# Performance work log

Hardware: AMD Instinct MI355X
Metric: run time of the kernel (lower is better)

## Reference

```python
import jax, jax.numpy as jnp
import numpy as np

B, T, D, H = 2, 2048, 1024, 16
DK = D // H


def setup_inputs() -> dict:
    key = jax.random.key(0)
    ks = jax.random.split(key, 12)
    s = 0.02
    return {
        "query": jax.random.normal(ks[0], (B, T, D), jnp.float32),
        "key": jax.random.normal(ks[1], (B, T, D), jnp.float32),
        "value": jax.random.normal(ks[2], (B, T, D), jnp.float32),
        "mask": jax.random.randint(ks[3], (B, T), 0, 2) != 0,  # True = keep
        "Wq": jax.random.normal(ks[4], (D, D), jnp.float32) * s,
        "bq": jnp.zeros((D,), jnp.float32),
        "Wk": jax.random.normal(ks[5], (D, D), jnp.float32) * s,
        "bk": jnp.zeros((D,), jnp.float32),
        "Wv": jax.random.normal(ks[6], (D, D), jnp.float32) * s,
        "bv": jnp.zeros((D,), jnp.float32),
        "Wo": jax.random.normal(ks[7], (D, D), jnp.float32) * s,
        "bo": jnp.zeros((D,), jnp.float32),
    }


def _split_heads(x):
    # [B, S, D] -> [B, H, S, DK]
    b, s, _ = x.shape
    return x.reshape(b, s, H, DK).transpose(0, 2, 1, 3)


def reference(query, key, value, mask, Wq, bq, Wk, bk, Wv, bv, Wo, bo):
    # torch Linear: y = x @ W.T + b
    q = _split_heads(query @ Wq.T + bq)   # [B,H,T,DK]
    k = _split_heads(key @ Wk.T + bk)     # [B,H,S,DK]
    v = _split_heads(value @ Wv.T + bv)   # [B,H,S,DK]
    scale = 1.0 / np.sqrt(DK).astype(np.float32)
    scores = jnp.einsum('bhtd,bhsd->bhts', q, k) * scale  # [B,H,T,S]
    # key-padding mask [B,S] -> broadcast [B,1,1,S], True = keep
    scores = jnp.where(mask[:, None, None, :], scores, -jnp.inf)
    attn = jax.nn.softmax(scores, axis=-1)
    out = jnp.einsum('bhts,bhsd->bhtd', attn, v)           # [B,H,T,DK]
    out = out.transpose(0, 2, 1, 3).reshape(query.shape[0], -1, D)
    return out @ Wo.T + bo
```

## Files before the change

kernel.cpp:

```cpp
#include <hip/hip_runtime.h>
#include <stdint.h>

#define B_SZ 2
#define T_SEQ 2048
#define DMODEL 1024
#define NHEAD 16
#define DKH 64
#define M_ROWS (B_SZ * T_SEQ)

#define LDT 72

#define INP_E  4194304u
#define W_E    1048576u

typedef __bf16 bf16x8 __attribute__((ext_vector_type(8)));
typedef float  f32x4  __attribute__((ext_vector_type(4)));

__device__ __forceinline__ unsigned short f2bf(float f) {
    unsigned u = __builtin_bit_cast(unsigned, f);
    u += 0x7fffu + ((u >> 16) & 1u);
    return (unsigned short)(u >> 16);
}
__device__ __forceinline__ uint4 cvt8(const float* p) {
    float4 f0 = *(const float4*)p, f1 = *(const float4*)(p + 4);
    uint4 r;
    r.x = (unsigned)f2bf(f0.x) | ((unsigned)f2bf(f0.y) << 16);
    r.y = (unsigned)f2bf(f0.z) | ((unsigned)f2bf(f0.w) << 16);
    r.z = (unsigned)f2bf(f1.x) | ((unsigned)f2bf(f1.y) << 16);
    r.w = (unsigned)f2bf(f1.z) | ((unsigned)f2bf(f1.w) << 16);
    return r;
}

__device__ __forceinline__ void async16(const unsigned short* g, unsigned short* l) {
    __builtin_amdgcn_global_load_lds(
        (const __attribute__((address_space(1))) void*)g,
        (__attribute__((address_space(3))) void*)l, 16, 0, 0);
}
__device__ __forceinline__ void async4(const unsigned short* g, unsigned short* l) {
    __builtin_amdgcn_global_load_lds(
        (const __attribute__((address_space(1))) void*)g,
        (__attribute__((address_space(3))) void*)l, 4, 0, 0);
}

__global__ __launch_bounds__(256) void cvt_all(
    const float* __restrict__ q, const float* __restrict__ k, const float* __restrict__ v,
    const float* __restrict__ wq, const float* __restrict__ wk,
    const float* __restrict__ wv, const float* __restrict__ wo,
    unsigned short* __restrict__ wsb)
{
    int blk = blockIdx.x;
    const float* src; unsigned short* dst; int lb;
    if      (blk < 2048) { src = q;  dst = wsb;                       lb = blk; }
    else if (blk < 4096) { src = k;  dst = wsb + INP_E;               lb = blk - 2048; }
    else if (blk < 6144) { src = v;  dst = wsb + 2 * INP_E;           lb = blk - 4096; }
    else if (blk < 6656) { src = wq; dst = wsb + 3 * INP_E;           lb = blk - 6144; }
    else if (blk < 7168) { src = wk; dst = wsb + 3 * INP_E + W_E;     lb = blk - 6656; }
    else if (blk < 7680) { src = wv; dst = wsb + 3 * INP_E + 2 * W_E; lb = blk - 7168; }
    else                 { src = wo; dst = wsb + 3 * INP_E + 3 * W_E; lb = blk - 7680; }
    size_t i = ((size_t)lb * 256 + threadIdx.x) * 8;
    *(uint4*)&dst[i] = cvt8(src + i);
}

template<int C_MODE, int MT>
__device__ __forceinline__ void gemm_core(
    const unsigned short* __restrict__ A, const unsigned short* __restrict__ W,
    const float* __restrict__ bias, void* __restrict__ C,
    int N, int K, int bx, int by,
    unsigned short* sA, unsigned short* sB)
{
    const int tid  = threadIdx.x;
    const int wave = tid >> 6, lane = tid & 63;
    const int quad = lane >> 4, l15 = lane & 15;
    const int TM = MT * 32;
    const int m0 = by * TM, n0 = bx * 128;
    const int wm = (wave & 1) * (MT * 16), wn = (wave >> 1) * 64;

    f32x4 acc[MT][4] = {};

    for (int k0 = 0; k0 < K; k0 += 64) {
        __syncthreads();
        #pragma unroll
        for (int i = 0; i < MT; i++) {
            int c   = tid + 256 * i;
            int row = c >> 3;
            int gk  = ((c & 7) ^ (row & 7)) * 8;
            int sb  = (wave * 64 + 256 * i) * 8;
            async16(&A[(size_t)(m0 + row) * K + k0 + gk], sA + sb);
        }
        #pragma unroll
        for (int i = 0; i < 4; i++) {
            int c   = tid + 256 * i;
            int row = c >> 3;
            int gk  = ((c & 7) ^ (row & 7)) * 8;
            int sb  = (wave * 64 + 256 * i) * 8;
            async16(&W[(size_t)(n0 + row) * K + k0 + gk], sB + sb);
        }
        __syncthreads();
        const int sw = l15 & 7;
        #pragma unroll
        for (int ks = 0; ks < 2; ks++) {
            bf16x8 af[MT], bfv[4];
            #pragma unroll
            for (int mt = 0; mt < MT; mt++)
                af[mt] = *(const bf16x8*)&sA[(wm + mt * 16 + l15) * 64 +
                                             (((ks * 4 + quad) ^ sw) * 8)];
            #pragma unroll
            for (int nt = 0; nt < 4; nt++)
                bfv[nt] = *(const bf16x8*)&sB[(wn + nt * 16 + l15) * 64 +
                                              (((ks * 4 + quad) ^ sw) * 8)];
            #pragma unroll
            for (int mt = 0; mt < MT; mt++)
                #pragma unroll
                for (int nt = 0; nt < 4; nt++)
                    acc[mt][nt] = __builtin_amdgcn_mfma_f32_16x16x32_bf16(
                        af[mt], bfv[nt], acc[mt][nt], 0, 0, 0);
        }
    }

    if (C_MODE == 2) {
        #pragma unroll
        for (int mt = 0; mt < MT; mt++) {
            #pragma unroll
            for (int r = 0; r < 4; r++) {
                int m = m0 + wm + mt * 16 + quad * 4 + r;
                float bm = bias[m];
                #pragma unroll
                for (int nt = 0; nt < 4; nt++) {
                    int n = n0 + wn + nt * 16 + l15;
                    int bb = n >> 11, t = n & 2047;
                    ((unsigned short*)C)[((size_t)bb * 1024 + m) * 2048 + t] =
                        f2bf(acc[mt][nt][r] + bm);
                }
            }
        }
    } else {
        #pragma unroll
        for (int nt = 0; nt < 4; nt++) {
            int n = n0 + wn + nt * 16 + l15;
            float bv = bias[n];
            #pragma unroll
            for (int mt = 0; mt < MT; mt++) {
                #pragma unroll
                for (int r = 0; r < 4; r++) {
                    int m = m0 + wm + mt * 16 + quad * 4 + r;
                    float val = acc[mt][nt][r] + bv;
                    if (C_MODE == 1) ((float*)C)[(size_t)m * N + n] = val;
                    else ((unsigned short*)C)[(size_t)m * N + n] = f2bf(val);
                }
            }
        }
    }
}

__global__ __launch_bounds__(256) void gemm_qkv(
    const unsigned short* __restrict__ Qb, const unsigned short* __restrict__ Kb,
    const unsigned short* __restrict__ Vb,
    const unsigned short* __restrict__ Wqb, const unsigned short* __restrict__ Wkb,
    const unsigned short* __restrict__ Wvb,
    const float* __restrict__ bq, const float* __restrict__ bk, const float* __restrict__ bv,
    unsigned short* __restrict__ Qp, unsigned short* __restrict__ Kp,
    unsigned short* __restrict__ Vt)
{
    __shared__ __align__(16) unsigned short sA[128 * 64];
    __shared__ __align__(16) unsigned short sB[128 * 64];
    const int z = blockIdx.z, id = blockIdx.x;
    if (z < 2) {
        gemm_core<0, 4>(z ? Kb : Qb, z ? Wkb : Wqb, z ? bk : bq, z ? Kp : Qp,
                        DMODEL, DMODEL, id & 7, id >> 3, sA, sB);
    } else {
        gemm_core<2, 4>(Wvb, Vb, bv, Vt, M_ROWS, DMODEL, id & 31, id >> 5, sA, sB);
    }
}

__global__ __launch_bounds__(256) void gemm_o(
    const unsigned short* __restrict__ AO, const unsigned short* __restrict__ Wob,
    const float* __restrict__ bo, float* __restrict__ out)
{
    __shared__ __align__(16) unsigned short sA[64 * 64];
    __shared__ __align__(16) unsigned short sB[128 * 64];
    const int id = blockIdx.x;
    gemm_core<1, 2>(AO, Wob, bo, out, DMODEL, DMODEL, id & 7, id >> 3, sA, sB);
}

#define QBLK 128
#define KVB 64

__global__ __launch_bounds__(512, 4) void attn_kernel(
    const unsigned short* __restrict__ Qp,
    const unsigned short* __restrict__ Kp,
    const unsigned short* __restrict__ Vt,
    const int* __restrict__ maskp,
    unsigned short* __restrict__ Op)
{
    __shared__ __align__(16) unsigned char sMEM[73728];
    unsigned short* sK  = (unsigned short*)sMEM;
    unsigned short* sV  = (unsigned short*)(sMEM + 32768);
    float*          smf = (float*)(sMEM + 65536);

    const int tid  = threadIdx.x;
    const int wave = tid >> 6, lane = tid & 63;
    const int g    = wave >> 2, wl = wave & 3;
    const int quad = lane >> 4, l15 = lane & 15;
    const int qblk = blockIdx.x, h = blockIdx.y, b = blockIdx.z;

    const float SCL2 = 0.125f * 1.44269504089f;
    const float MNEG = -30000.f;

    bf16x8 aq[2][2];
    #pragma unroll
    for (int mt = 0; mt < 2; mt++) {
        const int qrow = qblk * QBLK + wl * 32 + mt * 16 + l15;
        const unsigned short* qptr =
            Qp + (size_t)(b * T_SEQ + qrow) * DMODEL + h * DKH + quad * 8;
        aq[mt][0] = *(const bf16x8*)qptr;
        aq[mt][1] = *(const bf16x8*)(qptr + 32);
    }

    const unsigned short* Kb_ = Kp + (size_t)b * T_SEQ * DMODEL + h * DKH;
    const unsigned short* VtB = Vt + ((size_t)b * DMODEL + h * DKH) * T_SEQ;

    int kOff[2], kSb[2];
    #pragma unroll
    for (int i = 0; i < 2; i++) {
        int c = tid + 512 * i;
        int tile = c >> 9, cc = c & 511;
        int row = cc >> 3;
        int gk = ((cc & 7) ^ (row & 7)) * 8;
        kOff[i] = (tile * 64 + row) * DMODEL + gk;
        kSb[i]  = (wave * 64 + 512 * i) * 8;
    }
    int vOff[8], vSb[8];
    #pragma unroll
    for (int i = 0; i < 8; i++) {
        int P    = wave * 2048 + i * 256 + lane * 4;
        int tile = P >> 13;
        int rp   = P & 8191;
        int row  = rp >> 7;
        int cb   = (rp >> 4) & 7;
        int slot = (rp >> 2) & 3;
        int c    = cb ^ (row & 7);
        int f    = c * 4 + slot;
        int g2   = ((f >> 4) << 1) | ((f >> 1) & 1);
        int qq   = (f >> 2) & 3;
        int r2   = (f & 1) * 2;
        int keyoff = g2 * 16 + qq * 4 + r2;
        vOff[i] = row * T_SEQ + tile * 64 + keyoff;
        vSb[i]  = (wave * 2048 + i * 256) >> 1;
    }

    f32x4 O[2][4] = {};
    float l_r[2] = {0.f, 0.f};

    #pragma unroll
    for (int i = 0; i < 2; i++)
        async16(&Kb_[kOff[i]], sK + kSb[i]);
    #pragma unroll
    for (int i = 0; i < 8; i++)
        async4(&VtB[vOff[i]], sV + vSb[i]);
    #pragma unroll
    for (int j = 0; j < 4; j++) {
        int i = tid + 512 * j;
        smf[i] = maskp[b * T_SEQ + i] ? 0.f : MNEG;
    }
    __syncthreads();

    const int sw = l15 & 7;
    for (int rr = 0; rr < T_SEQ / (2 * KVB); ++rr) {
        const int cur = rr & 1;
        if (rr + 1 < T_SEQ / (2 * KVB)) {
            const int nb = cur ^ 1;
            #pragma unroll
            for (int i = 0; i < 2; i++)
                async16(&Kb_[(size_t)(rr + 1) * 128 * DMODEL + kOff[i]],
                        sK + nb * 8192 + kSb[i]);
            #pragma unroll
            for (int i = 0; i < 8; i++)
                async4(&VtB[(size_t)(rr + 1) * 128 + vOff[i]],
                       sV + nb * 8192 + vSb[i]);
        }

        const unsigned short* sKp = sK + cur * 8192 + g * 4096;
        const unsigned short* sVp = sV + cur * 8192 + g * 4096;
        const int s0 = (2 * rr + g) * KVB;

        f32x4 ST[2][4];
        __builtin_amdgcn_s_setprio(1);
        #pragma unroll
        for (int kt = 0; kt < 4; kt++) {
            const unsigned short* kr = &sKp[(kt * 16 + l15) * 64];
            const bf16x8 kf0 = *(const bf16x8*)&kr[(quad ^ sw) * 8];
            const bf16x8 kf1 = *(const bf16x8*)&kr[((quad + 4) ^ sw) * 8];
            #pragma unroll
            for (int mt = 0; mt < 2; mt++) {
                f32x4 z = {};
                z = __builtin_amdgcn_mfma_f32_16x16x32_bf16(kf0, aq[mt][0], z, 0, 0, 0);
                z = __builtin_amdgcn_mfma_f32_16x16x32_bf16(kf1, aq[mt][1], z, 0, 0, 0);
                ST[mt][kt] = z;
            }
        }
        __builtin_amdgcn_s_setprio(0);

        bf16x8 pb[2][2];
        #pragma unroll
        for (int kt = 0; kt < 4; kt++) {
            float4 m4 = *(const float4*)&smf[s0 + kt * 16 + quad * 4];
            float ma[4] = {m4.x, m4.y, m4.z, m4.w};
            #pragma unroll
            for (int mt = 0; mt < 2; mt++) {
                #pragma unroll
                for (int r = 0; r < 4; r++) {
                    float p = __builtin_amdgcn_exp2f(fmaf(ST[mt][kt][r], SCL2, ma[r]));
                    l_r[mt] += p;
                    pb[mt][kt >> 1][(kt & 1) * 4 + r] = (__bf16)p;
                }
            }
        }

        __builtin_amdgcn_s_setprio(1);
        #pragma unroll
        for (int nt = 0; nt < 4; nt++) {
            const unsigned short* vr = &sVp[(nt * 16 + l15) * 64];
            const bf16x8 vf0 = *(const bf16x8*)&vr[(quad ^ sw) * 8];
            const bf16x8 vf1 = *(const bf16x8*)&vr[((quad + 4) ^ sw) * 8];
            #pragma unroll
            for (int mt = 0; mt < 2; mt++) {
                O[mt][nt] = __builtin_amdgcn_mfma_f32_16x16x32_bf16(
                    vf0, pb[mt][0], O[mt][nt], 0, 0, 0);
                O[mt][nt] = __builtin_amdgcn_mfma_f32_16x16x32_bf16(
                    vf1, pb[mt][1], O[mt][nt], 0, 0, 0);
            }
        }
        __builtin_amdgcn_s_setprio(0);

        __syncthreads();
    }

    #pragma unroll
    for (int mt = 0; mt < 2; mt++) {
        float l = l_r[mt];
        l += __shfl_xor(l, 16);
        l += __shfl_xor(l, 32);
        l_r[mt] = l;
    }

    float* OM = (float*)sMEM;
    float* LM = (float*)(sMEM + 33280);
    if (g == 1) {
        #pragma unroll
        for (int mt = 0; mt < 2; mt++) {
            int row = wl * 32 + mt * 16 + l15;
            if (quad == 0) LM[row] = l_r[mt];
            #pragma unroll
            for (int nt = 0; nt < 4; nt++)
                #pragma unroll
                for (int r = 0; r < 4; r++)
                    OM[row * 65 + nt * 16 + quad * 4 + r] = O[mt][nt][r];
        }
    }
    __syncthreads();
    if (g == 0) {
        #pragma unroll
        for (int mt = 0; mt < 2; mt++) {
            int row = wl * 32 + mt * 16 + l15;
            float inv = 1.0f / fmaxf(l_r[mt] + LM[row], 1e-30f);
            int qg = qblk * QBLK + row;
            unsigned short* op = Op + (size_t)(b * T_SEQ + qg) * DMODEL + h * DKH;
            #pragma unroll
            for (int nt = 0; nt < 4; nt++) {
                ushort4 w;
                w.x = f2bf((O[mt][nt][0] + OM[row * 65 + nt * 16 + quad * 4 + 0]) * inv);
                w.y = f2bf((O[mt][nt][1] + OM[row * 65 + nt * 16 + quad * 4 + 1]) * inv);
                w.z = f2bf((O[mt][nt][2] + OM[row * 65 + nt * 16 + quad * 4 + 2]) * inv);
                w.w = f2bf((O[mt][nt][3] + OM[row * 65 + nt * 16 + quad * 4 + 3]) * inv);
                *(ushort4*)&op[nt * 16 + quad * 4] = w;
            }
        }
    }
}

template<int A_BF16, int W_BF16, int C_MODE>
__global__ __launch_bounds__(256) void gemm_bt_cvt(
    const void* __restrict__ A_, const void* __restrict__ W_,
    const float* __restrict__ bias, void* __restrict__ C_,
    int M, int N, int K)
{
    __shared__ __align__(16) unsigned short sA[128 * LDT];
    __shared__ __align__(16) unsigned short sB[128 * LDT];
    const int tid  = threadIdx.x;
    const int wave = tid >> 6, lane = tid & 63;
    const int quad = lane >> 4, l15 = lane & 15;
    const int m0 = blockIdx.y * 128, n0 = blockIdx.x * 128;
    const int wm = (wave & 1) * 64, wn = (wave >> 1) * 64;
    f32x4 acc[4][4] = {};
    for (int k0 = 0; k0 < K; k0 += 64) {
        __syncthreads();
        #pragma unroll
        for (int i = 0; i < 4; i++) {
            int c = tid + 256 * i;
            int row = c >> 3, koff = (c & 7) * 8;
            if (A_BF16)
                *(uint4*)&sA[row * LDT + koff] =
                    *(const uint4*)&((const unsigned short*)A_)[(size_t)(m0 + row) * K + k0 + koff];
            else
                *(uint4*)&sA[row * LDT + koff] =
                    cvt8((const float*)A_ + (size_t)(m0 + row) * K + k0 + koff);
            if (W_BF16)
                *(uint4*)&sB[row * LDT + koff] =
                    *(const uint4*)&((const unsigned short*)W_)[(size_t)(n0 + row) * K + k0 + koff];
            else
                *(uint4*)&sB[row * LDT + koff] =
                    cvt8((const float*)W_ + (size_t)(n0 + row) * K + k0 + koff);
        }
        __syncthreads();
        #pragma unroll
        for (int ks = 0; ks < 2; ks++) {
            bf16x8 af[4], bfr[4];
            #pragma unroll
            for (int mt = 0; mt < 4; mt++)
                af[mt] = *(const bf16x8*)&sA[(wm + mt * 16 + l15) * LDT + ks * 32 + quad * 8];
            #pragma unroll
            for (int nt = 0; nt < 4; nt++)
                bfr[nt] = *(const bf16x8*)&sB[(wn + nt * 16 + l15) * LDT + ks * 32 + quad * 8];
            #pragma unroll
            for (int mt = 0; mt < 4; mt++)
                #pragma unroll
                for (int nt = 0; nt < 4; nt++)
                    acc[mt][nt] = __builtin_amdgcn_mfma_f32_16x16x32_bf16(
                        af[mt], bfr[nt], acc[mt][nt], 0, 0, 0);
        }
    }
    if (C_MODE == 2) {
        #pragma unroll
        for (int mt = 0; mt < 4; mt++)
            #pragma unroll
            for (int r = 0; r < 4; r++) {
                int m = m0 + wm + mt * 16 + quad * 4 + r;
                float bm = bias[m];
                #pragma unroll
                for (int nt = 0; nt < 4; nt++) {
                    int n = n0 + wn + nt * 16 + l15;
                    int bb = n >> 11, t = n & 2047;
                    ((unsigned short*)C_)[((size_t)bb * 1024 + m) * 2048 + t] =
                        f2bf(acc[mt][nt][r] + bm);
                }
            }
    } else {
        #pragma unroll
        for (int nt = 0; nt < 4; nt++) {
            int n = n0 + wn + nt * 16 + l15;
            float bv = bias[n];
            #pragma unroll
            for (int mt = 0; mt < 4; mt++)
                #pragma unroll
                for (int r = 0; r < 4; r++) {
                    int m = m0 + wm + mt * 16 + quad * 4 + r;
                    float val = acc[mt][nt][r] + bv;
                    if (C_MODE == 1) ((float*)C_)[(size_t)m * N + n] = val;
                    else ((unsigned short*)C_)[(size_t)m * N + n] = f2bf(val);
                }
        }
    }
}

extern "C" void kernel_launch(void* const* d_in, const int* in_sizes, int n_in,
                              void* d_out, int out_size, void* d_ws, size_t ws_size,
                              hipStream_t stream)
{
    const float* q  = (const float*)d_in[0];
    const float* k  = (const float*)d_in[1];
    const float* v  = (const float*)d_in[2];
    const int*   mk = (const int*)d_in[3];
    const float* Wq = (const float*)d_in[4];
    const float* bq = (const float*)d_in[5];
    const float* Wk = (const float*)d_in[6];
    const float* bk = (const float*)d_in[7];
    const float* Wv = (const float*)d_in[8];
    const float* bv = (const float*)d_in[9];
    const float* Wo = (const float*)d_in[10];
    const float* bo = (const float*)d_in[11];
    float* out = (float*)d_out;

    unsigned short* wsb = (unsigned short*)d_ws;
    const dim3 gA(T_SEQ / QBLK, NHEAD, B_SZ);

    if (ws_size >= (size_t)64 * 1024 * 1024) {
        unsigned short* Qb  = wsb;
        unsigned short* Kb  = wsb + INP_E;
        unsigned short* Vb  = wsb + 2 * INP_E;
        unsigned short* Wqb = wsb + 3 * INP_E;
        unsigned short* Wkb = wsb + 3 * INP_E + W_E;
        unsigned short* Wvb = wsb + 3 * INP_E + 2 * W_E;
        unsigned short* Wob = wsb + 3 * INP_E + 3 * W_E;
        unsigned short* Qp  = wsb + 4 * INP_E;
        unsigned short* Kp  = wsb + 5 * INP_E;
        unsigned short* Vt  = wsb + 6 * INP_E;
        unsigned short* AO  = wsb + 7 * INP_E;

        cvt_all<<<8192, 256, 0, stream>>>(q, k, v, Wq, Wk, Wv, Wo, wsb);
        gemm_qkv<<<dim3(256, 1, 3), 256, 0, stream>>>(
            Qb, Kb, Vb, Wqb, Wkb, Wvb, bq, bk, bv, Qp, Kp, Vt);
        attn_kernel<<<gA, 512, 0, stream>>>(Qp, Kp, Vt, mk, AO);
        gemm_o<<<dim3(512, 1, 1), 256, 0, stream>>>(AO, Wob, bo, out);
    } else {
        unsigned short* Qp = wsb;
        unsigned short* Kp = wsb + INP_E;
        unsigned short* Vt = wsb + 2 * INP_E;
        unsigned short* AO = wsb + 3 * INP_E;
        const dim3 gN(DMODEL / 128, M_ROWS / 128);
        const dim3 gV(M_ROWS / 128, DMODEL / 128);
        gemm_bt_cvt<0, 0, 0><<<gN, 256, 0, stream>>>(q, Wq, bq, Qp, M_ROWS, DMODEL, DMODEL);
        gemm_bt_cvt<0, 0, 0><<<gN, 256, 0, stream>>>(k, Wk, bk, Kp, M_ROWS, DMODEL, DMODEL);
        gemm_bt_cvt<0, 0, 2><<<gV, 256, 0, stream>>>(Wv, v, bv, Vt, DMODEL, M_ROWS, DMODEL);
        attn_kernel<<<gA, 512, 0, stream>>>(Qp, Kp, Vt, mk, AO);
        gemm_bt_cvt<1, 0, 1><<<gN, 256, 0, stream>>>(AO, Wo, bo, out, M_ROWS, DMODEL, DMODEL);
    }
}
```

Baseline: 223.6 us.

## Widen attention block to 16 waves with four KV groups, single-buffered tiles

```diff
diff --git a/kernel.cpp b/kernel.cpp
--- a/kernel.cpp
+++ b/kernel.cpp
@@ -185,7 +185,7 @@
 #define QBLK 128
 #define KVB 64
 
-__global__ __launch_bounds__(512, 4) void attn_kernel(
+__global__ __launch_bounds__(1024, 8) void attn_kernel(
     const unsigned short* __restrict__ Qp,
     const unsigned short* __restrict__ Kp,
     const unsigned short* __restrict__ Vt,
@@ -222,30 +222,31 @@
     int kOff[2], kSb[2];
     #pragma unroll
     for (int i = 0; i < 2; i++) {
-        int c = tid + 512 * i;
+        int c = tid + 1024 * i;
         int tile = c >> 9, cc = c & 511;
         int row = cc >> 3;
         int gk = ((cc & 7) ^ (row & 7)) * 8;
         kOff[i] = (tile * 64 + row) * DMODEL + gk;
-        kSb[i]  = (wave * 64 + 512 * i) * 8;
+        kSb[i]  = (wave * 64 + 1024 * i) * 8;
     }
     int vOff[8], vSb[8];
     #pragma unroll
     for (int i = 0; i < 8; i++) {
-        int P    = wave * 2048 + i * 256 + lane * 4;
+        int c    = tid + 1024 * i;
+        int P    = c * 4;
         int tile = P >> 13;
         int rp   = P & 8191;
         int row  = rp >> 7;
         int cb   = (rp >> 4) & 7;
         int slot = (rp >> 2) & 3;
-        int c    = cb ^ (row & 7);
-        int f    = c * 4 + slot;
+        int cc2  = cb ^ (row & 7);
+        int f    = cc2 * 4 + slot;
         int g2   = ((f >> 4) << 1) | ((f >> 1) & 1);
         int qq   = (f >> 2) & 3;
         int r2   = (f & 1) * 2;
         int keyoff = g2 * 16 + qq * 4 + r2;
         vOff[i] = row * T_SEQ + tile * 64 + keyoff;
-        vSb[i]  = (wave * 2048 + i * 256) >> 1;
+        vSb[i]  = (wave * 64 + 1024 * i) * 2;
     }
 
     f32x4 O[2][4] = {};
@@ -258,30 +259,18 @@
     for (int i = 0; i < 8; i++)
         async4(&VtB[vOff[i]], sV + vSb[i]);
     #pragma unroll
-    for (int j = 0; j < 4; j++) {
-        int i = tid + 512 * j;
+    for (int j = 0; j < 2; j++) {
+        int i = tid + 1024 * j;
         smf[i] = maskp[b * T_SEQ + i] ? 0.f : MNEG;
     }
     __syncthreads();
 
     const int sw = l15 & 7;
-    for (int rr = 0; rr < T_SEQ / (2 * KVB); ++rr) {
-        const int cur = rr & 1;
-        if (rr + 1 < T_SEQ / (2 * KVB)) {
-            const int nb = cur ^ 1;
-            #pragma unroll
-            for (int i = 0; i < 2; i++)
-                async16(&Kb_[(size_t)(rr + 1) * 128 * DMODEL + kOff[i]],
-                        sK + nb * 8192 + kSb[i]);
-            #pragma unroll
-            for (int i = 0; i < 8; i++)
-                async4(&VtB[(size_t)(rr + 1) * 128 + vOff[i]],
-                       sV + nb * 8192 + vSb[i]);
-        }
-
-        const unsigned short* sKp = sK + cur * 8192 + g * 4096;
-        const unsigned short* sVp = sV + cur * 8192 + g * 4096;
-        const int s0 = (2 * rr + g) * KVB;
+    const unsigned short* sKp = sK + g * 4096;
+    const unsigned short* sVp = sV + g * 4096;
+
+    for (int rr = 0; rr < T_SEQ / (4 * KVB); ++rr) {
+        const int s0 = rr * 256 + g * KVB;
 
         f32x4 ST[2][4];
         __builtin_amdgcn_s_setprio(1);
@@ -333,6 +322,15 @@
         __builtin_amdgcn_s_setprio(0);
 
         __syncthreads();
+        if (rr + 1 < T_SEQ / (4 * KVB)) {
+            #pragma unroll
+            for (int i = 0; i < 2; i++)
+                async16(&Kb_[(size_t)(rr + 1) * 256 * DMODEL + kOff[i]], sK + kSb[i]);
+            #pragma unroll
+            for (int i = 0; i < 8; i++)
+                async4(&VtB[(size_t)(rr + 1) * 256 + vOff[i]], sV + vSb[i]);
+            __syncthreads();
+        }
     }
 
     #pragma unroll
@@ -343,9 +341,13 @@
         l_r[mt] = l;
     }
 
-    float* OM = (float*)sMEM;
-    float* LM = (float*)(sMEM + 33280);
-    if (g == 1) {
+    float* OM0 = (float*)sMEM;
+    float* OM1 = (float*)(sMEM + 33280);
+    float* LM0 = (float*)(sMEM + 66560);
+    float* LM1 = (float*)(sMEM + 67072);
+    if (g == 1 || g == 3) {
+        float* OM = (g == 1) ? OM0 : OM1;
+        float* LM = (g == 1) ? LM0 : LM1;
         #pragma unroll
         for (int mt = 0; mt < 2; mt++) {
             int row = wl * 32 + mt * 16 + l15;
@@ -358,20 +360,48 @@
         }
     }
     __syncthreads();
-    if (g == 0) {
+    if (g == 0 || g == 2) {
+        float* OM = (g == 0) ? OM0 : OM1;
+        float* LM = (g == 0) ? LM0 : LM1;
         #pragma unroll
         for (int mt = 0; mt < 2; mt++) {
             int row = wl * 32 + mt * 16 + l15;
-            float inv = 1.0f / fmaxf(l_r[mt] + LM[row], 1e-30f);
+            l_r[mt] += LM[row];
+            #pragma unroll
+            for (int nt = 0; nt < 4; nt++)
+                #pragma unroll
+                for (int r = 0; r < 4; r++)
+                    O[mt][nt][r] += OM[row * 65 + nt * 16 + quad * 4 + r];
+        }
+    }
+    __syncthreads();
+    if (g == 2) {
+        #pragma unroll
+        for (int mt = 0; mt < 2; mt++) {
+            int row = wl * 32 + mt * 16 + l15;
+            if (quad == 0) LM0[row] = l_r[mt];
+            #pragma unroll
+            for (int nt = 0; nt < 4; nt++)
+                #pragma unroll
+                for (int r = 0; r < 4; r++)
+                    OM0[row * 65 + nt * 16 + quad * 4 + r] = O[mt][nt][r];
+        }
+    }
+    __syncthreads();
+    if (g == 0) {
+        #pragma unroll
+        for (int mt = 0; mt < 2; mt++) {
+            int row = wl * 32 + mt * 16 + l15;
+            float inv = 1.0f / fmaxf(l_r[mt] + LM0[row], 1e-30f);
             int qg = qblk * QBLK + row;
             unsigned short* op = Op + (size_t)(b * T_SEQ + qg) * DMODEL + h * DKH;
             #pragma unroll
             for (int nt = 0; nt < 4; nt++) {
                 ushort4 w;
-                w.x = f2bf((O[mt][nt][0] + OM[row * 65 + nt * 16 + quad * 4 + 0]) * inv);
-                w.y = f2bf((O[mt][nt][1] + OM[row * 65 + nt * 16 + quad * 4 + 1]) * inv);
-                w.z = f2bf((O[mt][nt][2] + OM[row * 65 + nt * 16 + quad * 4 + 2]) * inv);
-                w.w = f2bf((O[mt][nt][3] + OM[row * 65 + nt * 16 + quad * 4 + 3]) * inv);
+                w.x = f2bf((O[mt][nt][0] + OM0[row * 65 + nt * 16 + quad * 4 + 0]) * inv);
+                w.y = f2bf((O[mt][nt][1] + OM0[row * 65 + nt * 16 + quad * 4 + 1]) * inv);
+                w.z = f2bf((O[mt][nt][2] + OM0[row * 65 + nt * 16 + quad * 4 + 2]) * inv);
+                w.w = f2bf((O[mt][nt][3] + OM0[row * 65 + nt * 16 + quad * 4 + 3]) * inv);
                 *(ushort4*)&op[nt * 16 + quad * 4] = w;
             }
         }
@@ -499,7 +529,7 @@
         cvt_all<<<8192, 256, 0, stream>>>(q, k, v, Wq, Wk, Wv, Wo, wsb);
         gemm_qkv<<<dim3(256, 1, 3), 256, 0, stream>>>(
             Qb, Kb, Vb, Wqb, Wkb, Wvb, bq, bk, bv, Qp, Kp, Vt);
-        attn_kernel<<<gA, 512, 0, stream>>>(Qp, Kp, Vt, mk, AO);
+        attn_kernel<<<gA, 1024, 0, stream>>>(Qp, Kp, Vt, mk, AO);
         gemm_o<<<dim3(512, 1, 1), 256, 0, stream>>>(AO, Wob, bo, out);
     } else {
         unsigned short* Qp = wsb;
@@ -511,7 +541,7 @@
         gemm_bt_cvt<0, 0, 0><<<gN, 256, 0, stream>>>(q, Wq, bq, Qp, M_ROWS, DMODEL, DMODEL);
         gemm_bt_cvt<0, 0, 0><<<gN, 256, 0, stream>>>(k, Wk, bk, Kp, M_ROWS, DMODEL, DMODEL);
         gemm_bt_cvt<0, 0, 2><<<gV, 256, 0, stream>>>(Wv, v, bv, Vt, DMODEL, M_ROWS, DMODEL);
-        attn_kernel<<<gA, 512, 0, stream>>>(Qp, Kp, Vt, mk, AO);
+        attn_kernel<<<gA, 1024, 0, stream>>>(Qp, Kp, Vt, mk, AO);
         gemm_bt_cvt<1, 0, 1><<<gN, 256, 0, stream>>>(AO, Wo, bo, out, M_ROWS, DMODEL, DMODEL);
     }
 }
```

Result: slower. 551.5 us (+146.7%).
